# Optimization experiments

Measured on AMD Instinct MI355X. Metric: run time of the kernel, lower is better.

Reference implementation:

```python
import jax, jax.numpy as jnp
import numpy as np

N = 128       # n_channels
B = 131072    # batch
C = np.float32(np.sqrt(0.5))  # 50/50 beamsplitter amplitude (c = s = sqrt(0.5))


def setup_inputs() -> dict:
    key = jax.random.key(0)
    k1, k2, k3, k4 = jax.random.split(key, 4)
    M = N * (N - 1) // 2
    return {
        "x_real": jax.random.normal(k1, (B, N), jnp.float32),
        "x_imag": jax.random.normal(k2, (B, N), jnp.float32),
        "mzi_phases": jax.random.normal(k3, (M * 2,), jnp.float32) * 0.1,
        "output_phases": jax.random.normal(k4, (N,), jnp.float32) * 0.1,
    }


def _construct_unitary(mzi_phases, output_phases):
    n = output_phases.shape[0]
    m = n * (n - 1) // 2
    # pair ordering matches the torch double loop: i ascending, then j > i (row-major triu)
    i_np, j_np = np.triu_indices(n, 1)
    i_idx = jnp.asarray(i_np, jnp.int32)
    j_idx = jnp.asarray(j_np, jnp.int32)
    ph = mzi_phases.reshape(m, 2)
    theta, phi = ph[:, 0], ph[:, 1]

    def step(U, xs):
        th, ph_, i, j = xs
        e_phi = jax.lax.complex(jnp.cos(ph_), jnp.sin(ph_))
        e_th = jax.lax.complex(jnp.cos(th), jnp.sin(th))
        ri = U[i]
        rj = U[j]
        # T_ij @ U touches only rows i and j (O(N) Givens row update)
        new_i = C * ri + (C * e_phi) * rj
        new_j = (C * e_th) * ri - (C * e_th * e_phi) * rj
        U = U.at[i].set(new_i).at[j].set(new_j)
        return U, None

    def chunk_body(U, xs_chunk):
        U, _ = jax.lax.scan(step, U, xs_chunk)
        return U, None

    # chunk the M sequential updates: M = (n-1) * (n//2) for even n;
    # checkpointing chunks keeps reverse-mode memory O(sqrt-ish) instead of O(M * N^2)
    n_chunks = n - 1
    cs = n // 2
    xs = (theta.reshape(n_chunks, cs), phi.reshape(n_chunks, cs),
          i_idx.reshape(n_chunks, cs), j_idx.reshape(n_chunks, cs))
    U0 = jnp.eye(n, dtype=jnp.complex64)
    U, _ = jax.lax.scan(jax.checkpoint(chunk_body), U0, xs)
    # output phase screen D @ U
    d = jax.lax.complex(jnp.cos(output_phases), jnp.sin(output_phases))
    return d[:, None] * U


def reference(x_real, x_imag, mzi_phases, output_phases):
    U = _construct_unitary(mzi_phases, output_phases)           # [N, N] complex64
    x = jax.lax.complex(x_real, x_imag)                          # [B, N] complex64
    # matmul(U, x.unsqueeze(-1)).squeeze(-1) == x @ U^T
    out = jnp.einsum('nm,bm->bn', U, x)                          # [B, N] complex64
    # ComplexDropout is identity in eval mode
    return out
```

## Files before the change

kernel.cpp:

```cpp
#include <hip/hip_runtime.h>
#include <hip/hip_bf16.h>

#define NDIM 128
#define BDIM 131072
#define NMZI 8128
#define NCHUNK 8
#define CSTEP (NMZI / NCHUNK)
#define NJG 8
#define NCOL 32
#define NLOC 16
static constexpr float CC = 0.70710678118654752440f;

typedef __attribute__((ext_vector_type(8))) short bf16x8;
typedef __attribute__((ext_vector_type(4))) float f32x4;

__device__ __align__(16) float2         g_V[NCHUNK * NDIM * NDIM];
__device__ __align__(16) float2         g_W[4 * NDIM * NDIM];
__device__ __align__(16) float2         g_Y[2 * NDIM * NDIM];
__device__ __align__(16) unsigned short g_TB[32 * NDIM * 8];
__device__ __align__(16) unsigned short g_Ur[16 * NDIM * 8];
__device__ __align__(16) unsigned short g_Ui[16 * NDIM * 8];

__device__ inline unsigned short f2bf(float f) {
    union { __hip_bfloat16 h; unsigned short u; } cv;
    cv.h = __float2bfloat16(f);
    return cv.u;
}

__global__ __launch_bounds__(256) void build_scan(const float* __restrict__ mzi) {
    __shared__ float2 Usm[NDIM][NCOL];
    __shared__ float4 phs[CSTEP];
    __shared__ float4 comp[NJG][NCOL];
    const int tid   = threadIdx.x;
    const int c     = tid & 31;
    const int g     = tid >> 5;
    const int col0  = blockIdx.x * NCOL;
    const int chunk = blockIdx.y;
    const int s0 = chunk * CSTEP, s1 = s0 + CSTEP;

    for (int k = g; k < NDIM; k += NJG)
        Usm[k][c] = make_float2((k == col0 + c) ? 1.f : 0.f, 0.f);
    const float2* mzp = (const float2*)mzi;
    for (int t = tid; t < CSTEP; t += 256) {
        const float2 mz = mzp[s0 + t];
        float sp, cp, st, ct;
        sincosf(mz.y, &sp, &cp);
        sincosf(mz.x, &st, &ct);
        phs[t] = make_float4(cp, sp, CC * ct, CC * st);
    }
    __syncthreads();

    int i = 0, base = 0;
    while (base + (NDIM - 1 - i) <= s0) { base += NDIM - 1 - i; ++i; }

    int s = s0;
    while (s < s1) {
        const int cnt  = NDIM - 1 - i;
        const int jA   = i + 1 + (s - base);
        const int L    = min(s1, base + cnt) - s;
        const int nloc = (L + NJG - 1) >> 3;
        const int myBeg = g * nloc;
        const int myN   = max(0, min(nloc, L - myBeg));
        const int pbase = s - s0;

        const float2 r0 = Usm[i][c];

        float2 treg[NLOC];
        float2 qth[NLOC];
        float  A = 1.f;
        float2 Bc = make_float2(0.f, 0.f);
        #pragma unroll
        for (int kk = 0; kk < NLOC; ++kk) {
            if (kk < myN) {
                const int off = myBeg + kk;
                const float4 q  = phs[pbase + off];
                const float2 rj = Usm[jA + off][c];
                const float tr = fmaf(q.x, rj.x, -q.y * rj.y);
                const float ti = fmaf(q.x, rj.y,  q.y * rj.x);
                treg[kk] = make_float2(tr, ti);
                qth[kk]  = make_float2(q.z, q.w);
                Bc.x = CC * (Bc.x + tr);
                Bc.y = CC * (Bc.y + ti);
                A *= CC;
            }
        }
        comp[g][c] = make_float4(A, Bc.x, Bc.y, 0.f);
        __syncthreads();

        float2 r = r0;
        for (int h = 0; h < g; ++h) {
            const float4 cm = comp[h][c];
            r.x = fmaf(cm.x, r.x, cm.y);
            r.y = fmaf(cm.x, r.y, cm.z);
        }

        #pragma unroll
        for (int kk = 0; kk < NLOC; ++kk) {
            if (kk < myN) {
                const float2 t = treg[kk];
                const float2 q = qth[kk];
                const float dr = r.x - t.x, di = r.y - t.y;
                const float njx = fmaf(q.x, dr, -q.y * di);
                const float njy = fmaf(q.x, di,  q.y * dr);
                Usm[jA + myBeg + kk][c] = make_float2(njx, njy);
                r.x = CC * (r.x + t.x);
                r.y = CC * (r.y + t.y);
            }
        }
        if (myN > 0 && (myBeg + myN == L))
            Usm[i][c] = r;
        __syncthreads();

        s += L;
        if (s == base + cnt) { base += cnt; ++i; }
    }

    float2* Vp = g_V + chunk * NDIM * NDIM;
    for (int k = g; k < NDIM; k += NJG)
        Vp[k * NDIM + col0 + c] = Usm[k][c];
}

__global__ __launch_bounds__(128) void compose(int level) {
    const int p = blockIdx.y, n = blockIdx.x, m = threadIdx.x;
    const float2* A; const float2* B; float2* Cout;
    if (level == 0) {
        A = g_V + (2 * p + 1) * NDIM * NDIM;
        B = g_V + (2 * p) * NDIM * NDIM;
        Cout = g_W + p * NDIM * NDIM;
    } else {
        A = g_W + (2 * p + 1) * NDIM * NDIM;
        B = g_W + (2 * p) * NDIM * NDIM;
        Cout = g_Y + p * NDIM * NDIM;
    }
    __shared__ float2 arow[NDIM];
    arow[m] = A[n * NDIM + m];
    __syncthreads();
    float cr = 0.f, ci = 0.f;
    #pragma unroll 8
    for (int k = 0; k < NDIM; ++k) {
        const float2 b = B[k * NDIM + m];
        const float2 a = arow[k];
        cr = fmaf(a.x, b.x, fmaf(-a.y, b.y, cr));
        ci = fmaf(a.x, b.y, fmaf( a.y, b.x, ci));
    }
    Cout[n * NDIM + m] = make_float2(cr, ci);
}

__global__ __launch_bounds__(128) void compose_final(const float* __restrict__ oph) {
    const int n = blockIdx.x, m = threadIdx.x;
    const float2* A = g_Y + NDIM * NDIM;
    const float2* B = g_Y;
    __shared__ float2 arow[NDIM];
    arow[m] = A[n * NDIM + m];
    __syncthreads();
    float cr = 0.f, ci = 0.f;
    #pragma unroll 8
    for (int k = 0; k < NDIM; ++k) {
        const float2 b = B[k * NDIM + m];
        const float2 a = arow[k];
        cr = fmaf(a.x, b.x, fmaf(-a.y, b.y, cr));
        ci = fmaf(a.x, b.y, fmaf( a.y, b.x, ci));
    }
    float ds, dc;
    sincosf(oph[n], &ds, &dc);
    const float vr = fmaf(cr, dc, -ci * ds);
    const float vi = fmaf(cr, ds,  ci * dc);
    const int kg = m >> 3, e = m & 7;
    g_TB[(kg * NDIM + n) * 8 + e]        = f2bf(vr);
    g_TB[((16 + kg) * NDIM + n) * 8 + e] = f2bf(-vi);
    g_Ur[(kg * NDIM + n) * 8 + e] = f2bf(vr);
    g_Ui[(kg * NDIM + n) * 8 + e] = f2bf(vi);
}

__global__ __launch_bounds__(256) void cmatmul0(const float* __restrict__ xr,
                                                const float* __restrict__ xi,
                                                float* __restrict__ out) {
    __shared__ __align__(16) char smX[4][8192];
    const int tid  = threadIdx.x;
    const int lane = tid & 63;
    const int w    = tid >> 6;
    const int r15  = lane & 15;
    const int kg4  = lane >> 4;
    const int l31  = lane & 31;
    const int lh   = lane >> 5;
    const int R    = blockIdx.x * 64 + w * 16;

    const float4* sre = (const float4*)(xr + (size_t)R * NDIM);
    const float4* sim = (const float4*)(xi + (size_t)R * NDIM);
    float4 G[16];
    #pragma unroll
    for (int p = 0; p < 8; ++p) G[p]     = sre[p * 64 + lane];
    #pragma unroll
    for (int p = 0; p < 8; ++p) G[8 + p] = sim[p * 64 + lane];

    char* buf = &smX[w][0];
    #pragma unroll
    for (int p = 0; p < 8; ++p) {
        const int row = 2 * p + lh;
        const int swz = (row & 7) << 4;
        uint2 v;
        v.x = ((unsigned)f2bf(G[p].y) << 16) | f2bf(G[p].x);
        v.y = ((unsigned)f2bf(G[p].w) << 16) | f2bf(G[p].z);
        *(uint2*)(buf + row * 512 + ((l31 * 8) ^ swz)) = v;
        v.x = ((unsigned)f2bf(G[8 + p].y) << 16) | f2bf(G[8 + p].x);
        v.y = ((unsigned)f2bf(G[8 + p].w) << 16) | f2bf(G[8 + p].z);
        *(uint2*)(buf + row * 512 + 256 + ((l31 * 8) ^ swz)) = v;
    }

    bf16x8 fx[8];
    const int rswz = (r15 & 7) << 4;
    #pragma unroll
    for (int kc = 0; kc < 8; ++kc) {
        const int off = (((kc & 3) * 64 + kg4 * 16) ^ rswz) + ((kc >= 4) ? 256 : 0);
        fx[kc] = *(const bf16x8*)(buf + r15 * 512 + off);
    }

    const bf16x8* gT = (const bf16x8*)g_TB;
    const size_t orow = (size_t)(R + r15) * NDIM;
    #pragma unroll
    for (int nt = 0; nt < 8; ++nt) {
        f32x4 a0 = {0.f, 0.f, 0.f, 0.f};
        f32x4 a1 = {0.f, 0.f, 0.f, 0.f};
        #pragma unroll
        for (int kc = 0; kc < 4; ++kc)
            a0 = __builtin_amdgcn_mfma_f32_16x16x32_bf16(
                gT[(kc * 4 + kg4) * NDIM + nt * 16 + r15], fx[kc], a0, 0, 0, 0);
        #pragma unroll
        for (int kc = 4; kc < 8; ++kc)
            a1 = __builtin_amdgcn_mfma_f32_16x16x32_bf16(
                gT[(kc * 4 + kg4) * NDIM + nt * 16 + r15], fx[kc], a1, 0, 0, 0);
        const f32x4 s = a0 + a1;
        *(float4*)(out + orow + nt * 16 + kg4 * 4) =
            make_float4(s[0], s[1], s[2], s[3]);
    }
}

__global__ __launch_bounds__(256) void cmatmul1(const float* __restrict__ xr,
                                                const float* __restrict__ xi,
                                                ushort2* __restrict__ outp) {
    const int lane  = threadIdx.x & 63;
    const int w     = threadIdx.x >> 6;
    const int btile = blockIdx.x * 64 + w * 16;
    const int r15   = lane & 15;
    const int kg4   = lane >> 4;
    const int bload = btile + r15;

    const bf16x8* Ur = (const bf16x8*)g_Ur;
    const bf16x8* Ui = (const bf16x8*)g_Ui;
    const float* xrp = xr + (size_t)bload * NDIM;
    const float* xip = xi + (size_t)bload * NDIM;

    bf16x8 ar[4], ai[4], ain[4];
    #pragma unroll
    for (int kc = 0; kc < 4; ++kc) {
        const int k0 = kc * 32 + kg4 * 8;
        float4 rlo = *(const float4*)(xrp + k0);
        float4 rhi = *(const float4*)(xrp + k0 + 4);
        float4 ilo = *(const float4*)(xip + k0);
        float4 ihi = *(const float4*)(xip + k0 + 4);
        bf16x8 vr, vi, vn;
        vr[0] = (short)f2bf(rlo.x); vr[1] = (short)f2bf(rlo.y);
        vr[2] = (short)f2bf(rlo.z); vr[3] = (short)f2bf(rlo.w);
        vr[4] = (short)f2bf(rhi.x); vr[5] = (short)f2bf(rhi.y);
        vr[6] = (short)f2bf(rhi.z); vr[7] = (short)f2bf(rhi.w);
        vi[0] = (short)f2bf(ilo.x); vi[1] = (short)f2bf(ilo.y);
        vi[2] = (short)f2bf(ilo.z); vi[3] = (short)f2bf(ilo.w);
        vi[4] = (short)f2bf(ihi.x); vi[5] = (short)f2bf(ihi.y);
        vi[6] = (short)f2bf(ihi.z); vi[7] = (short)f2bf(ihi.w);
        #pragma unroll
        for (int e = 0; e < 8; ++e) vn[e] = (short)(vi[e] ^ 0x8000);
        ar[kc] = vr; ai[kc] = vi; ain[kc] = vn;
    }

    #pragma unroll
    for (int nt = 0; nt < 8; ++nt) {
        f32x4 accR = {0.f, 0.f, 0.f, 0.f};
        f32x4 accI = {0.f, 0.f, 0.f, 0.f};
        #pragma unroll
        for (int kc = 0; kc < 4; ++kc) {
            const int kg = kc * 4 + kg4;
            bf16x8 br = Ur[kg * NDIM + nt * 16 + r15];
            bf16x8 bi = Ui[kg * NDIM + nt * 16 + r15];
            accR = __builtin_amdgcn_mfma_f32_16x16x32_bf16(ar[kc],  br, accR, 0, 0, 0);
            accR = __builtin_amdgcn_mfma_f32_16x16x32_bf16(ain[kc], bi, accR, 0, 0, 0);
            accI = __builtin_amdgcn_mfma_f32_16x16x32_bf16(ar[kc],  bi, accI, 0, 0, 0);
            accI = __builtin_amdgcn_mfma_f32_16x16x32_bf16(ai[kc],  br, accI, 0, 0, 0);
        }
        const int n    = nt * 16 + r15;
        const int brow = btile + kg4 * 4;
        #pragma unroll
        for (int r = 0; r < 4; ++r)
            outp[(size_t)(brow + r) * NDIM + n] = make_ushort2(f2bf(accR[r]), f2bf(accI[r]));
    }
}

extern "C" void kernel_launch(void* const* d_in, const int* in_sizes, int n_in,
                              void* d_out, int out_size, void* d_ws, size_t ws_size,
                              hipStream_t stream) {
    const float* xr  = (const float*)d_in[0];
    const float* xi  = (const float*)d_in[1];
    const float* mzi = (const float*)d_in[2];
    const float* oph = (const float*)d_in[3];

    build_scan<<<dim3(4, NCHUNK), dim3(256), 0, stream>>>(mzi);
    compose<<<dim3(NDIM, 4), dim3(128), 0, stream>>>(0);
    compose<<<dim3(NDIM, 2), dim3(128), 0, stream>>>(1);
    compose_final<<<dim3(NDIM), dim3(128), 0, stream>>>(oph);
    if (out_size == BDIM * NDIM) {
        cmatmul0<<<dim3(BDIM / 64), dim3(256), 0, stream>>>(xr, xi, (float*)d_out);
    } else {
        cmatmul1<<<dim3(BDIM / 64), dim3(256), 0, stream>>>(xr, xi, (ushort2*)d_out);
    }
}
```

Measured before the change: 122.7 us.

## Split build scan by row sweeps with double-buffered phases; stage matmul output through LDS

```diff
diff --git a/kernel.cpp b/kernel.cpp
--- a/kernel.cpp
+++ b/kernel.cpp
@@ -5,7 +5,6 @@
 #define BDIM 131072
 #define NMZI 8128
 #define NCHUNK 8
-#define CSTEP (NMZI / NCHUNK)
 #define NJG 8
 #define NCOL 32
 #define NLOC 16
@@ -29,41 +28,47 @@
 
 __global__ __launch_bounds__(256) void build_scan(const float* __restrict__ mzi) {
     __shared__ float2 Usm[NDIM][NCOL];
-    __shared__ float4 phs[CSTEP];
+    __shared__ float4 ph[2][NDIM];
     __shared__ float4 comp[NJG][NCOL];
     const int tid   = threadIdx.x;
     const int c     = tid & 31;
     const int g     = tid >> 5;
     const int col0  = blockIdx.x * NCOL;
     const int chunk = blockIdx.y;
-    const int s0 = chunk * CSTEP, s1 = s0 + CSTEP;
+    const int i0    = chunk * 16;
 
     for (int k = g; k < NDIM; k += NJG)
         Usm[k][c] = make_float2((k == col0 + c) ? 1.f : 0.f, 0.f);
+
     const float2* mzp = (const float2*)mzi;
-    for (int t = tid; t < CSTEP; t += 256) {
-        const float2 mz = mzp[s0 + t];
-        float sp, cp, st, ct;
-        sincosf(mz.y, &sp, &cp);
-        sincosf(mz.x, &st, &ct);
-        phs[t] = make_float4(cp, sp, CC * ct, CC * st);
+    int base = 127 * i0 - (i0 * (i0 - 1)) / 2;
+    {
+        const int L0 = NDIM - 1 - i0;
+        if (tid < L0) {
+            const float2 mz = mzp[base + tid];
+            float sp, cp, st, ct;
+            sincosf(mz.y, &sp, &cp);
+            sincosf(mz.x, &st, &ct);
+            ph[0][tid] = make_float4(cp, sp, CC * ct, CC * st);
+        }
     }
     __syncthreads();
 
-    int i = 0, base = 0;
-    while (base + (NDIM - 1 - i) <= s0) { base += NDIM - 1 - i; ++i; }
-
-    int s = s0;
-    while (s < s1) {
-        const int cnt  = NDIM - 1 - i;
-        const int jA   = i + 1 + (s - base);
-        const int L    = min(s1, base + cnt) - s;
-        const int nloc = (L + NJG - 1) >> 3;
+    #pragma unroll 1
+    for (int sw = 0; sw < 16; ++sw) {
+        const int i = i0 + sw;
+        const int L = NDIM - 1 - i;
+        if (L <= 0) break;
+        const int cur = sw & 1;
+
+        float2 mznext;
+        const bool have = (sw < 15) && (tid < L - 1);
+        if (have) mznext = mzp[base + L + tid];
+
+        const float2 r0 = Usm[i][c];
+        const int nloc  = (L + NJG - 1) >> 3;
         const int myBeg = g * nloc;
         const int myN   = max(0, min(nloc, L - myBeg));
-        const int pbase = s - s0;
-
-        const float2 r0 = Usm[i][c];
 
         float2 treg[NLOC];
         float2 qth[NLOC];
@@ -73,8 +78,8 @@
         for (int kk = 0; kk < NLOC; ++kk) {
             if (kk < myN) {
                 const int off = myBeg + kk;
-                const float4 q  = phs[pbase + off];
-                const float2 rj = Usm[jA + off][c];
+                const float4 q  = ph[cur][off];
+                const float2 rj = Usm[i + 1 + off][c];
                 const float tr = fmaf(q.x, rj.x, -q.y * rj.y);
                 const float ti = fmaf(q.x, rj.y,  q.y * rj.x);
                 treg[kk] = make_float2(tr, ti);
@@ -102,17 +107,22 @@
                 const float dr = r.x - t.x, di = r.y - t.y;
                 const float njx = fmaf(q.x, dr, -q.y * di);
                 const float njy = fmaf(q.x, di,  q.y * dr);
-                Usm[jA + myBeg + kk][c] = make_float2(njx, njy);
+                Usm[i + 1 + myBeg + kk][c] = make_float2(njx, njy);
                 r.x = CC * (r.x + t.x);
                 r.y = CC * (r.y + t.y);
             }
         }
         if (myN > 0 && (myBeg + myN == L))
             Usm[i][c] = r;
+
+        if (have) {
+            float sp, cp, st, ct;
+            sincosf(mznext.y, &sp, &cp);
+            sincosf(mznext.x, &st, &ct);
+            ph[cur ^ 1][tid] = make_float4(cp, sp, CC * ct, CC * st);
+        }
         __syncthreads();
-
-        s += L;
-        if (s == base + cnt) { base += cnt; ++i; }
+        base += L;
     }
 
     float2* Vp = g_V + chunk * NDIM * NDIM;
@@ -185,13 +195,13 @@
     const int lh   = lane >> 5;
     const int R    = blockIdx.x * 64 + w * 16;
 
-    const float4* sre = (const float4*)(xr + (size_t)R * NDIM);
-    const float4* sim = (const float4*)(xi + (size_t)R * NDIM);
-    float4 G[16];
-    #pragma unroll
-    for (int p = 0; p < 8; ++p) G[p]     = sre[p * 64 + lane];
-    #pragma unroll
-    for (int p = 0; p < 8; ++p) G[8 + p] = sim[p * 64 + lane];
+    const f32x4* sre = (const f32x4*)(xr + (size_t)R * NDIM);
+    const f32x4* sim = (const f32x4*)(xi + (size_t)R * NDIM);
+    f32x4 G[16];
+    #pragma unroll
+    for (int p = 0; p < 8; ++p) G[p]     = __builtin_nontemporal_load(sre + p * 64 + lane);
+    #pragma unroll
+    for (int p = 0; p < 8; ++p) G[8 + p] = __builtin_nontemporal_load(sim + p * 64 + lane);
 
     char* buf = &smX[w][0];
     #pragma unroll
@@ -199,11 +209,11 @@
         const int row = 2 * p + lh;
         const int swz = (row & 7) << 4;
         uint2 v;
-        v.x = ((unsigned)f2bf(G[p].y) << 16) | f2bf(G[p].x);
-        v.y = ((unsigned)f2bf(G[p].w) << 16) | f2bf(G[p].z);
+        v.x = ((unsigned)f2bf(G[p][1]) << 16) | f2bf(G[p][0]);
+        v.y = ((unsigned)f2bf(G[p][3]) << 16) | f2bf(G[p][2]);
         *(uint2*)(buf + row * 512 + ((l31 * 8) ^ swz)) = v;
-        v.x = ((unsigned)f2bf(G[8 + p].y) << 16) | f2bf(G[8 + p].x);
-        v.y = ((unsigned)f2bf(G[8 + p].w) << 16) | f2bf(G[8 + p].z);
+        v.x = ((unsigned)f2bf(G[8 + p][1]) << 16) | f2bf(G[8 + p][0]);
+        v.y = ((unsigned)f2bf(G[8 + p][3]) << 16) | f2bf(G[8 + p][2]);
         *(uint2*)(buf + row * 512 + 256 + ((l31 * 8) ^ swz)) = v;
     }
 
@@ -216,7 +226,6 @@
     }
 
     const bf16x8* gT = (const bf16x8*)g_TB;
-    const size_t orow = (size_t)(R + r15) * NDIM;
     #pragma unroll
     for (int nt = 0; nt < 8; ++nt) {
         f32x4 a0 = {0.f, 0.f, 0.f, 0.f};
@@ -230,8 +239,17 @@
             a1 = __builtin_amdgcn_mfma_f32_16x16x32_bf16(
                 gT[(kc * 4 + kg4) * NDIM + nt * 16 + r15], fx[kc], a1, 0, 0, 0);
         const f32x4 s = a0 + a1;
-        *(float4*)(out + orow + nt * 16 + kg4 * 4) =
-            make_float4(s[0], s[1], s[2], s[3]);
+        *(f32x4*)(buf + r15 * 512 + ((nt * 64 + kg4 * 16) ^ rswz)) = s;
+    }
+
+    char* outp = (char*)(out + (size_t)R * NDIM);
+    #pragma unroll
+    for (int p = 0; p < 8; ++p) {
+        const int bofs = p * 1024 + lane * 16;
+        const int row  = bofs >> 9;
+        const int colb = bofs & 511;
+        const f32x4 v = *(const f32x4*)(buf + row * 512 + (colb ^ ((row & 7) << 4)));
+        __builtin_nontemporal_store(v, (f32x4*)(outp + bofs));
     }
 }
 
```

After: 108.8 us. 11.3% less time.
